# Kernel tuning notes

Measured on AMD Instinct MI355X. Metric: run time of the kernel, lower is better.

## Reference

```python
import jax, jax.numpy as jnp
import numpy as np

ALPHA = 0.7
N = 4194304
NUM_ACTIONS = 3


def setup_inputs() -> dict:
    key = jax.random.key(0)
    k1, k2, k3, k4, k5 = jax.random.split(key, 5)
    return {
        "pred_prices": jax.random.normal(k1, (N,), dtype=jnp.float32),
        "pred_actions": jax.random.normal(k2, (N, NUM_ACTIONS), dtype=jnp.float32),
        "tgt_prices": jax.random.normal(k3, (N,), dtype=jnp.float32),
        "tgt_actions": jax.random.randint(k4, (N,), 0, NUM_ACTIONS, dtype=jnp.int64),
        "prices": jax.random.normal(k5, (N,), dtype=jnp.float32),
    }


def reference(pred_prices, pred_actions, tgt_prices, tgt_actions, prices):
    # MSE over price predictions
    price_loss = jnp.mean((pred_prices - tgt_prices) ** 2)

    # Cross-entropy (mean over batch), matches nn.CrossEntropyLoss on logits
    logp = jax.nn.log_softmax(pred_actions, axis=-1)  # [N, 3]
    action_loss = -jnp.mean(jnp.take_along_axis(logp, tgt_actions[:, None], axis=-1))

    # Vectorized replacement of the per-sample profit loop (no_grad in original)
    predicted_actions = jnp.argmax(pred_actions, axis=-1)  # [N]
    p = tgt_prices
    d = p[1:] - p[:-1]                     # [N-1]
    zero = jnp.zeros((1,), p.dtype)
    diff_fwd = jnp.concatenate([d, zero])  # p[i+1]-p[i], last entry 0
    diff_bwd = jnp.concatenate([zero, d])  # p[i]-p[i-1], first entry 0
    profits = jnp.where(predicted_actions == 0, diff_fwd,
                        jnp.where(predicted_actions == 2, diff_bwd,
                                  jnp.zeros_like(p)))
    profit_weight = jax.nn.sigmoid(profits * 10.0)
    weighted_action_loss = action_loss * jnp.mean(profit_weight)

    return ALPHA * weighted_action_loss + (1.0 - ALPHA) * price_loss
```

## Files before the change

### kernel.cpp

```cpp
#include <hip/hip_runtime.h>

static constexpr int NN  = 4194304;
static constexpr int NB  = 4096;
static constexpr int TPB = 256;

__global__ __launch_bounds__(256) void pfl_main(
    const float* __restrict__ pp,
    const float* __restrict__ pa,
    const float* __restrict__ tp,
    const int*   __restrict__ ta,
    float* __restrict__ bsum)
{
    const int tid = threadIdx.x;
    const int bid = blockIdx.x;
    const int g   = bid * TPB + tid;
    const int i   = g * 4;

    const float4* pp4 = (const float4*)pp;
    const float4* tp4 = (const float4*)tp;
    const float4* pa4 = (const float4*)pa;
    const int4*   ta4 = (const int4*)ta;

    float4 p  = pp4[g];
    float4 t  = tp4[g];
    int4   a  = ta4[g];
    float4 A0 = pa4[3*g + 0];
    float4 A1 = pa4[3*g + 1];
    float4 A2 = pa4[3*g + 2];
    float tm1 = (i > 0)      ? tp[i - 1] : 0.f;
    float tnx = (i + 4 < NN) ? tp[i + 4] : 0.f;

    float tv[6] = {tm1, t.x, t.y, t.z, t.w, tnx};
    float pv[4] = {p.x, p.y, p.z, p.w};
    float rows[4][3] = {{A0.x, A0.y, A0.z},
                        {A0.w, A1.x, A1.y},
                        {A1.z, A1.w, A2.x},
                        {A2.y, A2.z, A2.w}};
    int av[4] = {a.x, a.y, a.z, a.w};

    float sq = 0.f, ce = 0.f, pw = 0.f;

    #pragma unroll
    for (int j = 0; j < 4; ++j) {
        const int idx = i + j;
        float d = pv[j] - tv[j + 1];
        sq += d * d;

        float x0 = rows[j][0], x1 = rows[j][1], x2 = rows[j][2];
        float m  = fmaxf(x0, fmaxf(x1, x2));
        float lse = m + __logf(__expf(x0 - m) + __expf(x1 - m) + __expf(x2 - m));
        float tgt = (av[j] == 0) ? x0 : ((av[j] == 1) ? x1 : x2);
        ce += lse - tgt;

        int pidx = 0;
        float best = x0;
        if (x1 > best) { best = x1; pidx = 1; }
        if (x2 > best) { pidx = 2; }

        float profit = 0.f;
        if (pidx == 0)      profit = (idx + 1 < NN) ? (tv[j + 2] - tv[j + 1]) : 0.f;
        else if (pidx == 2) profit = (idx > 0)      ? (tv[j + 1] - tv[j])     : 0.f;

        pw += 1.f / (1.f + __expf(-10.f * profit));
    }

    #pragma unroll
    for (int off = 32; off > 0; off >>= 1) {
        sq += __shfl_down(sq, off, 64);
        ce += __shfl_down(ce, off, 64);
        pw += __shfl_down(pw, off, 64);
    }

    __shared__ float s_sq[4], s_ce[4], s_pw[4];
    const int lane = tid & 63;
    const int wid  = tid >> 6;
    if (lane == 0) { s_sq[wid] = sq; s_ce[wid] = ce; s_pw[wid] = pw; }
    __syncthreads();

    if (tid == 0) {
        bsum[bid]          = s_sq[0] + s_sq[1] + s_sq[2] + s_sq[3];
        bsum[NB + bid]     = s_ce[0] + s_ce[1] + s_ce[2] + s_ce[3];
        bsum[2 * NB + bid] = s_pw[0] + s_pw[1] + s_pw[2] + s_pw[3];
    }
}

__global__ __launch_bounds__(1024) void pfl_final(const float* __restrict__ bsum,
                                                  float* __restrict__ out) {
    const int tid = threadIdx.x;
    const float4* b4 = (const float4*)bsum;
    const int Q = NB / 4;

    float4 vsq = b4[tid];
    float4 vce = b4[Q + tid];
    float4 vpw = b4[2 * Q + tid];

    double sq = (double)vsq.x + vsq.y + vsq.z + vsq.w;
    double ce = (double)vce.x + vce.y + vce.z + vce.w;
    double pw = (double)vpw.x + vpw.y + vpw.z + vpw.w;

    #pragma unroll
    for (int off = 32; off > 0; off >>= 1) {
        sq += __shfl_down(sq, off, 64);
        ce += __shfl_down(ce, off, 64);
        pw += __shfl_down(pw, off, 64);
    }

    __shared__ double s_sq[16], s_ce[16], s_pw[16];
    const int lane = tid & 63;
    const int wid  = tid >> 6;
    if (lane == 0) { s_sq[wid] = sq; s_ce[wid] = ce; s_pw[wid] = pw; }
    __syncthreads();

    if (tid == 0) {
        double tsq = 0.0, tce = 0.0, tpw = 0.0;
        #pragma unroll
        for (int w = 0; w < 16; ++w) { tsq += s_sq[w]; tce += s_ce[w]; tpw += s_pw[w]; }
        const double inv = 1.0 / (double)NN;
        out[0] = (float)(0.7 * (tce * inv) * (tpw * inv) + 0.3 * (tsq * inv));
    }
}

extern "C" void kernel_launch(void* const* d_in, const int* in_sizes, int n_in,
                              void* d_out, int out_size, void* d_ws, size_t ws_size,
                              hipStream_t stream) {
    const float* pp = (const float*)d_in[0];
    const float* pa = (const float*)d_in[1];
    const float* tp = (const float*)d_in[2];
    const int*   ta = (const int*)d_in[3];

    float* bsum = (float*)d_ws;

    pfl_main<<<NB, TPB, 0, stream>>>(pp, pa, tp, ta, bsum);
    pfl_final<<<1, 1024, 0, stream>>>(bsum, (float*)d_out);
}
```

Measured before the change: 135.1 us.

## Fuse final reduction into main kernel via last-block atomic counters

Removes the second reduction kernel launch. Each block publishes its partial sums with agent-scope stores, then bumps a two-level atomic counter (per group of 64 blocks, then a global one). The last block to finish reads all partials and writes the final loss. This saves a launch and its dependency gap, but adds an atomic per block and a serialized tail in the final block.

New measurement: 153.4 us. +13.6%, slower.

```diff
diff --git a/kernel.cpp b/kernel.cpp
--- a/kernel.cpp
+++ b/kernel.cpp
@@ -4,12 +4,21 @@
 static constexpr int NB  = 4096;
 static constexpr int TPB = 256;
 
+
+__device__ int g_cnt[65] = {0};
+
+#define ST_AGENT(pp_, v_) \
+    __hip_atomic_store((pp_), (v_), __ATOMIC_RELAXED, __HIP_MEMORY_SCOPE_AGENT)
+#define LD_AGENT(pp_) \
+    __hip_atomic_load((pp_), __ATOMIC_RELAXED, __HIP_MEMORY_SCOPE_AGENT)
+
 __global__ __launch_bounds__(256) void pfl_main(
     const float* __restrict__ pp,
     const float* __restrict__ pa,
     const float* __restrict__ tp,
     const int*   __restrict__ ta,
-    float* __restrict__ bsum)
+    float* __restrict__ bsum,
+    float* __restrict__ out)
 {
     const int tid = threadIdx.x;
     const int bid = blockIdx.x;
@@ -72,51 +81,65 @@
     }
 
     __shared__ float s_sq[4], s_ce[4], s_pw[4];
+    __shared__ int   s_last;
     const int lane = tid & 63;
     const int wid  = tid >> 6;
     if (lane == 0) { s_sq[wid] = sq; s_ce[wid] = ce; s_pw[wid] = pw; }
     __syncthreads();
 
     if (tid == 0) {
-        bsum[bid]          = s_sq[0] + s_sq[1] + s_sq[2] + s_sq[3];
-        bsum[NB + bid]     = s_ce[0] + s_ce[1] + s_ce[2] + s_ce[3];
-        bsum[2 * NB + bid] = s_pw[0] + s_pw[1] + s_pw[2] + s_pw[3];
+        float bsq = s_sq[0] + s_sq[1] + s_sq[2] + s_sq[3];
+        float bce = s_ce[0] + s_ce[1] + s_ce[2] + s_ce[3];
+        float bpw = s_pw[0] + s_pw[1] + s_pw[2] + s_pw[3];
+
+        ST_AGENT(&bsum[bid],          bsq);
+        ST_AGENT(&bsum[NB + bid],     bce);
+        ST_AGENT(&bsum[2 * NB + bid], bpw);
+        asm volatile("s_waitcnt vmcnt(0)" ::: "memory");
+
+        int last = 0;
+        const int grp  = bid >> 6;
+        const int oldg = atomicAdd(&g_cnt[grp], 1);
+        if (oldg == 63) {
+            ST_AGENT(&g_cnt[grp], 0);
+            const int oldm = atomicAdd(&g_cnt[64], 1);
+            if (oldm == 63) {
+                ST_AGENT(&g_cnt[64], 0);
+                last = 1;
+            }
+        }
+        s_last = last;
     }
-}
-
-__global__ __launch_bounds__(1024) void pfl_final(const float* __restrict__ bsum,
-                                                  float* __restrict__ out) {
-    const int tid = threadIdx.x;
-    const float4* b4 = (const float4*)bsum;
-    const int Q = NB / 4;
-
-    float4 vsq = b4[tid];
-    float4 vce = b4[Q + tid];
-    float4 vpw = b4[2 * Q + tid];
-
-    double sq = (double)vsq.x + vsq.y + vsq.z + vsq.w;
-    double ce = (double)vce.x + vce.y + vce.z + vce.w;
-    double pw = (double)vpw.x + vpw.y + vpw.z + vpw.w;
-
-    #pragma unroll
-    for (int off = 32; off > 0; off >>= 1) {
-        sq += __shfl_down(sq, off, 64);
-        ce += __shfl_down(ce, off, 64);
-        pw += __shfl_down(pw, off, 64);
-    }
-
-    __shared__ double s_sq[16], s_ce[16], s_pw[16];
-    const int lane = tid & 63;
-    const int wid  = tid >> 6;
-    if (lane == 0) { s_sq[wid] = sq; s_ce[wid] = ce; s_pw[wid] = pw; }
     __syncthreads();
 
-    if (tid == 0) {
-        double tsq = 0.0, tce = 0.0, tpw = 0.0;
+    if (s_last) {
+        double fsq = 0.0, fce = 0.0, fpw = 0.0;
+        const int base = tid * 16;
+        #pragma unroll 4
+        for (int k = 0; k < 16; ++k) {
+            fsq += (double)LD_AGENT(&bsum[base + k]);
+            fce += (double)LD_AGENT(&bsum[NB + base + k]);
+            fpw += (double)LD_AGENT(&bsum[2 * NB + base + k]);
+        }
+
         #pragma unroll
-        for (int w = 0; w < 16; ++w) { tsq += s_sq[w]; tce += s_ce[w]; tpw += s_pw[w]; }
-        const double inv = 1.0 / (double)NN;
-        out[0] = (float)(0.7 * (tce * inv) * (tpw * inv) + 0.3 * (tsq * inv));
+        for (int off = 32; off > 0; off >>= 1) {
+            fsq += __shfl_down(fsq, off, 64);
+            fce += __shfl_down(fce, off, 64);
+            fpw += __shfl_down(fpw, off, 64);
+        }
+
+        __shared__ double d_sq[4], d_ce[4], d_pw[4];
+        if (lane == 0) { d_sq[wid] = fsq; d_ce[wid] = fce; d_pw[wid] = fpw; }
+        __syncthreads();
+
+        if (tid == 0) {
+            double tsq = d_sq[0] + d_sq[1] + d_sq[2] + d_sq[3];
+            double tce = d_ce[0] + d_ce[1] + d_ce[2] + d_ce[3];
+            double tpw = d_pw[0] + d_pw[1] + d_pw[2] + d_pw[3];
+            const double inv = 1.0 / (double)NN;
+            out[0] = (float)(0.7 * (tce * inv) * (tpw * inv) + 0.3 * (tsq * inv));
+        }
     }
 }
 
@@ -130,6 +153,5 @@
 
     float* bsum = (float*)d_ws;
 
-    pfl_main<<<NB, TPB, 0, stream>>>(pp, pa, tp, ta, bsum);
-    pfl_final<<<1, 1024, 0, stream>>>(bsum, (float*)d_out);
+    pfl_main<<<NB, TPB, 0, stream>>>(pp, pa, tp, ta, bsum, (float*)d_out);
 }
```
